# Optimization experiments

Hardware: AMD Instinct MI355X
Metric: run time of the kernel (lower is better)

Reference implementation:

```python
import jax, jax.numpy as jnp
import numpy as np

N = 50000
E = 800000
NFEAT = 128
NHID = 32
HEADS = 8
NCLASS = 40


def _gat_conv(x, src, dst, W, att_src, att_dst, bias, concat):
    # x: [N, Fin]; W: [Fin, H*C]; att_*: [H, C]; bias: [H*C] or [C]
    n = x.shape[0]
    H, C = att_src.shape
    h = (x @ W).reshape(n, H, C)                      # [N,H,C]
    a_src = (h * att_src[None]).sum(-1)               # [N,H]
    a_dst = (h * att_dst[None]).sum(-1)               # [N,H]
    e = jax.nn.leaky_relu(a_src[src] + a_dst[dst], 0.2)  # [E,H]
    # edge softmax over incoming edges of each dst node
    m = jax.ops.segment_max(e, dst, num_segments=n)   # [N,H]
    e = jnp.exp(e - m[dst])
    s = jax.ops.segment_sum(e, dst, num_segments=n)   # [N,H]
    alpha = e / (s[dst] + 1e-16)                      # [E,H]
    msg = h[src] * alpha[:, :, None]                  # [E,H,C]
    out = jax.ops.segment_sum(msg, dst, num_segments=n)  # [N,H,C]
    if concat:
        out = out.reshape(n, H * C)
    else:
        out = out.mean(axis=1)
    return out + bias


def setup_inputs() -> dict:
    key = jax.random.key(0)
    ks = jax.random.split(key, 10)
    x = jax.random.normal(ks[0], (N, NFEAT), dtype=jnp.float32)
    edge_index = jax.random.randint(ks[1], (2, E), 0, N, dtype=jnp.int64)
    sc = 1.0 / np.sqrt(NFEAT)
    W1 = jax.random.uniform(ks[2], (NFEAT, HEADS * NHID), jnp.float32, -sc, sc)
    a1_src = jax.random.uniform(ks[3], (HEADS, NHID), jnp.float32, -sc, sc)
    a1_dst = jax.random.uniform(ks[4], (HEADS, NHID), jnp.float32, -sc, sc)
    b1 = jnp.zeros((HEADS * NHID,), jnp.float32)
    sc2 = 1.0 / np.sqrt(HEADS * NHID)
    W2 = jax.random.uniform(ks[5], (HEADS * NHID, NCLASS), jnp.float32, -sc2, sc2)
    a2_src = jax.random.uniform(ks[6], (1, NCLASS), jnp.float32, -sc2, sc2)
    a2_dst = jax.random.uniform(ks[7], (1, NCLASS), jnp.float32, -sc2, sc2)
    b2 = jnp.zeros((NCLASS,), jnp.float32)
    return {"x": x, "edge_index": edge_index, "W1": W1, "a1_src": a1_src,
            "a1_dst": a1_dst, "b1": b1, "W2": W2, "a2_src": a2_src,
            "a2_dst": a2_dst, "b2": b2}


def reference(x, edge_index, W1, a1_src, a1_dst, b1, W2, a2_src, a2_dst, b2):
    n = x.shape[0]
    loop = jnp.arange(n, dtype=edge_index.dtype)
    src = jnp.concatenate([edge_index[0], loop])  # add self-loops (PyG default)
    dst = jnp.concatenate([edge_index[1], loop])
    # dropout layers are identity in eval mode
    h = jax.nn.elu(_gat_conv(x, src, dst, W1, a1_src, a1_dst, b1, concat=True))
    out = _gat_conv(h, src, dst, W2, a2_src, a2_dst, b2, concat=False)
    return jax.nn.log_softmax(out, axis=1)
```

## Files before the change

### kernel.cpp

```cpp
#include <hip/hip_runtime.h>
#include <math.h>

#define NFEAT  128
#define HC     256
#define HEADS  8
#define NHID   32
#define NCLASS 40

#define INV_LN2 1.44269504088896340736f

typedef unsigned int  uint;
typedef unsigned short ushort;
typedef unsigned char uchar;

typedef __attribute__((ext_vector_type(8))) short bf16x8;
typedef __attribute__((ext_vector_type(4))) float f32x4;

union U8 { uint4 u; bf16x8 v; };

__device__ __forceinline__ uint f2bf1(float f) {
    uint b = __float_as_uint(f);
    b += 0x7FFFu + ((b >> 16) & 1u);
    return b >> 16;
}
__device__ __forceinline__ uint packbf(float lo, float hi) {
    return f2bf1(lo) | (f2bf1(hi) << 16);
}

__device__ __forceinline__ uchar f2fp8(float v) {
    return (uchar)(__builtin_amdgcn_cvt_pk_fp8_f32(v, v, 0, false) & 0xFF);
}
__device__ __forceinline__ float fp8tof(uint byte) {
    auto v2 = __builtin_amdgcn_cvt_pk_f32_fp8((int)byte, false);
    return v2[0];
}

__device__ __forceinline__ float bperm(int addr, float v) {
    return __int_as_float(__builtin_amdgcn_ds_bpermute(addr, __float_as_int(v)));
}


#define HU 4
#define PREPB 23
__global__ __launch_bounds__(256)
void k_hist_prep(const int* __restrict__ srcE, const int* __restrict__ dstE,
                 int E, int* deg, int* __restrict__ srcs,
                 const float* __restrict__ W1,
                 const float* __restrict__ attS, const float* __restrict__ attD,
                 const float* __restrict__ W2,
                 const float* __restrict__ a2sw, const float* __restrict__ a2dw,
                 ushort* __restrict__ Wb1, ushort* __restrict__ Wb2) {
    int blk = blockIdx.x;
    int t = threadIdx.x;
    if (blk >= PREPB) {
        int tid = (blk - PREPB) * 256 + t;
        int stride = (gridDim.x - PREPB) * 256;
#pragma unroll
        for (int j = 0; j < HU; ++j) {
            int i = tid + j * stride;
            if (i < E) {
                int d = dstE[i];
                int slot = atomicAdd(&deg[d], 1);
                if (slot < 64) srcs[((size_t)d << 6) + slot] = srcE[i];
            }
        }
        return;
    }
    float f[8];
    if (blk < 17) {
        int g = blk * 256 + t;
        int lane = g & 63;
        int step = (g >> 6) & 3;
        int tile = g >> 8;
        int k0 = step * 32 + (lane >> 4) * 8;
        if (tile < 16) {
            int ncol = tile * 16 + (lane & 15);
#pragma unroll
            for (int j = 0; j < 8; ++j) f[j] = W1[(size_t)(k0 + j) * HC + ncol];
        } else {
            int cc = lane & 15;
            int h = cc & 7;
            const float* av = (cc < 8) ? attS : attD;
#pragma unroll
            for (int j = 0; j < 8; ++j) {
                const float* wr = W1 + (size_t)(k0 + j) * HC + h * 32;
                float s = 0.f;
#pragma unroll
                for (int c = 0; c < 32; ++c) s += wr[c] * av[h * 32 + c];
                f[j] = s * INV_LN2;
            }
        }
        uint4 o;
        o.x = packbf(f[0], f[1]);
        o.y = packbf(f[2], f[3]);
        o.z = packbf(f[4], f[5]);
        o.w = packbf(f[6], f[7]);
        *(uint4*)(Wb1 + (size_t)g * 8) = o;
    } else {
        int g = (blk - 17) * 256 + t;
        if (g >= 3 * 8 * 64) return;
        int lane = g & 63;
        int ks = (g >> 6) & 7;
        int nt = g >> 9;
        int cc = lane & 15;
        int ncol = nt * 16 + cc;
        int k0 = ks * 32 + (lane >> 4) * 8;
        if (ncol < NCLASS) {
#pragma unroll
            for (int j = 0; j < 8; ++j) f[j] = W2[(size_t)(k0 + j) * NCLASS + ncol];
        } else if (ncol <= 41) {
            const float* av = (ncol == 40) ? a2sw : a2dw;
#pragma unroll
            for (int j = 0; j < 8; ++j) {
                const float* wr = W2 + (size_t)(k0 + j) * NCLASS;
                float s = 0.f;
#pragma unroll
                for (int c = 0; c < NCLASS; ++c) s += wr[c] * av[c];
                f[j] = s * INV_LN2;
            }
        } else {
#pragma unroll
            for (int j = 0; j < 8; ++j) f[j] = 0.f;
        }
        uint4 o;
        o.x = packbf(f[0], f[1]);
        o.y = packbf(f[2], f[3]);
        o.z = packbf(f[4], f[5]);
        o.w = packbf(f[6], f[7]);
        *(uint4*)(Wb2 + (size_t)g * 8) = o;
    }
}

__global__ __launch_bounds__(256)
void k_gemm1(const float* __restrict__ x, const ushort* __restrict__ Wb,
             int n, uchar* __restrict__ h1f8, float* __restrict__ a1x) {
    __shared__ uint Xs[64 * 68];
    int t = threadIdx.x;
    int lane = t & 63;
    int w = t >> 6;
    int n0 = blockIdx.x * 64;

#pragma unroll
    for (int j = 0; j < 8; ++j) {
        int f4 = t + j * 256;
        int node = f4 >> 5;
        int k4 = (f4 & 31) * 4;
        int gn = n0 + node;
        float4 v = make_float4(0.f, 0.f, 0.f, 0.f);
        if (gn < n) v = *(const float4*)(x + (size_t)gn * NFEAT + k4);
        uint2 pk;
        pk.x = packbf(v.x, v.y);
        pk.y = packbf(v.z, v.w);
        *(uint2*)(Xs + node * 68 + (k4 >> 1)) = pk;
    }
    __syncthreads();

    int m = lane & 15;
    int q4 = (lane >> 4) * 4;
    bf16x8 Af[4];
#pragma unroll
    for (int ks = 0; ks < 4; ++ks) {
        U8 a;
        a.u = *(const uint4*)(Xs + (w * 16 + m) * 68 + ks * 16 + q4);
        Af[ks] = a.v;
    }
    __syncthreads();

    f32x4 acc[17];
#pragma unroll
    for (int i = 0; i < 17; ++i) acc[i] = (f32x4){0.f, 0.f, 0.f, 0.f};

    const bf16x8* Bf = (const bf16x8*)Wb;
#pragma unroll
    for (int ks = 0; ks < 4; ++ks) {
#pragma unroll
        for (int nt = 0; nt < 17; ++nt) {
            bf16x8 bv = Bf[(size_t)(nt * 4 + ks) * 64 + lane];
            acc[nt] = __builtin_amdgcn_mfma_f32_16x16x32_bf16(Af[ks], bv, acc[nt], 0, 0, 0);
        }
    }

    int cc = lane & 15;
    int r0 = (lane >> 4) * 4;

#pragma unroll
    for (int r = 0; r < 4; ++r) {
        int gn = n0 + w * 16 + r0 + r;
        if (gn < n) a1x[(size_t)gn * 16 + cc] = acc[16][r];
    }

    uchar* CsB = (uchar*)Xs;
#pragma unroll
    for (int nt = 0; nt < 16; ++nt) {
#pragma unroll
        for (int r = 0; r < 4; ++r)
            CsB[(w * 16 + r0 + r) * 272 + nt * 16 + cc] = f2fp8(acc[nt][r]);
    }
    __syncthreads();

    int node_local = t >> 2;
    int q = t & 3;
    int gn = n0 + node_local;
    if (gn < n) {
        const uchar* crow = CsB + node_local * 272 + q * 64;
        uchar* hp = h1f8 + (size_t)gn * HC + q * 64;
#pragma unroll
        for (int i = 0; i < 4; ++i)
            *(uint4*)(hp + i * 16) = *(const uint4*)(crow + i * 16);
    }
}

__global__ __launch_bounds__(256)
void k_agg1(const uint* __restrict__ h1u, const float* __restrict__ a1x,
            const float* __restrict__ b1, const int* __restrict__ deg,
            const int* __restrict__ srcs,
            int n, ushort* __restrict__ hgb) {
    int wid = blockIdx.x * 4 + (threadIdx.x >> 6);
    if (wid >= n) return;
    wid = __builtin_amdgcn_readfirstlane(wid);
    int lane = threadIdx.x & 63;
    int vj = lane >> 3;
    int hh = lane & 7;
    int hacc = lane >> 3;
    float adn = a1x[(size_t)wid * 16 + 8 + hh];
    const char* a1xb = (const char*)a1x;
    int ax8  = (lane ^ 8)  << 2;
    int ax16 = (lane ^ 16) << 2;
    int ax32 = (lane ^ 32) << 2;
    int bpc  = hacc << 2;
    int bpp[8];
#pragma unroll
    for (int j = 0; j < 8; ++j) bpp[j] = ((j << 3) + hacc) << 2;

    int degw = __builtin_amdgcn_readfirstlane(deg[wid]);
    degw = (degw < 63) ? degw : 63;
    int cnt = degw + 1;
    const int* srow = srcs + ((size_t)wid << 6);

    float s = 0.f;
    float4 acc = make_float4(0.f, 0.f, 0.f, 0.f);

    for (int i = 0; i < cnt; i += 8) {
        int idx = i + vj;
        int ldi = (idx < degw) ? idx : 0;
        int lv = srow[ldi];
        int sv = (idx < degw) ? lv : wid;
        bool valid = idx < cnt;
        float av = *(const float*)(a1xb + ((size_t)(uint)sv << 6) + ((uint)hh << 2));
        float a = av + adn;
        float e = fmaxf(a, 0.2f * a);
        float p = valid ? __builtin_exp2f(e) : 0.f;
        s += p;
#pragma unroll
        for (int j = 0; j < 8; ++j) {
            int snj = srow[i + j];
            snj = ((i + j) < degw) ? snj : wid;
            uint hv = h1u[(size_t)snj * 64 + lane];
            float pj = bperm(bpp[j], p);
            auto lo = __builtin_amdgcn_cvt_pk_f32_fp8((int)hv, false);
            auto hi = __builtin_amdgcn_cvt_pk_f32_fp8((int)hv, true);
            acc.x += pj * lo[0];
            acc.y += pj * lo[1];
            acc.z += pj * hi[0];
            acc.w += pj * hi[1];
        }
    }

    float ps = s + bperm(ax8, s);
    ps += bperm(ax16, ps);
    ps += bperm(ax32, ps);
    float inv = 1.f / (ps + 1e-16f);
    float inv_a = bperm(bpc, inv);
    float4 bv = *(const float4*)(b1 + lane * 4);
    float4 o;
    o.x = acc.x * inv_a + bv.x;
    o.y = acc.y * inv_a + bv.y;
    o.z = acc.z * inv_a + bv.z;
    o.w = acc.w * inv_a + bv.w;
    o.x = (o.x > 0.f) ? o.x : (__expf(o.x) - 1.f);
    o.y = (o.y > 0.f) ? o.y : (__expf(o.y) - 1.f);
    o.z = (o.z > 0.f) ? o.z : (__expf(o.z) - 1.f);
    o.w = (o.w > 0.f) ? o.w : (__expf(o.w) - 1.f);
    uint2 ov;
    ov.x = packbf(o.x, o.y);
    ov.y = packbf(o.z, o.w);
    *(uint2*)(hgb + (size_t)wid * HC + lane * 4) = ov;
}

__global__ __launch_bounds__(256)
void k_gemm2(const ushort* __restrict__ hgb, const ushort* __restrict__ Wb2,
             int n, uchar* __restrict__ h2f8) {
    __shared__ uint Xs[64 * 132];
    int t = threadIdx.x;
    int lane = t & 63;
    int w = t >> 6;
    int n0 = blockIdx.x * 64;

#pragma unroll
    for (int j = 0; j < 8; ++j) {
        int g = t + j * 256;
        int node = g >> 5;
        int u4 = g & 31;
        int gn = n0 + node;
        uint4 v = make_uint4(0u, 0u, 0u, 0u);
        if (gn < n) v = *(const uint4*)(hgb + (size_t)gn * HC + u4 * 8);
        *(uint4*)(Xs + node * 132 + u4 * 4) = v;
    }
    __syncthreads();

    int m = lane & 15;
    int q4 = (lane >> 4) * 4;
    bf16x8 Af[8];
#pragma unroll
    for (int ks = 0; ks < 8; ++ks) {
        U8 a;
        a.u = *(const uint4*)(Xs + (w * 16 + m) * 132 + ks * 16 + q4);
        Af[ks] = a.v;
    }
    __syncthreads();

    f32x4 acc[3];
#pragma unroll
    for (int i = 0; i < 3; ++i) acc[i] = (f32x4){0.f, 0.f, 0.f, 0.f};

    const bf16x8* Bf = (const bf16x8*)Wb2;
#pragma unroll
    for (int ks = 0; ks < 8; ++ks) {
#pragma unroll
        for (int nt = 0; nt < 3; ++nt) {
            bf16x8 bv = Bf[(size_t)(nt * 8 + ks) * 64 + lane];
            acc[nt] = __builtin_amdgcn_mfma_f32_16x16x32_bf16(Af[ks], bv, acc[nt], 0, 0, 0);
        }
    }

    int cc = lane & 15;
    int r0 = (lane >> 4) * 4;

    uchar* CsB = (uchar*)Xs;
#pragma unroll
    for (int nt = 0; nt < 2; ++nt) {
#pragma unroll
        for (int r = 0; r < 4; ++r)
            CsB[(w * 16 + r0 + r) * 64 + nt * 16 + cc] = f2fp8(acc[nt][r]);
    }
#pragma unroll
    for (int r = 0; r < 4; ++r) {
        int row = (w * 16 + r0 + r) * 64;
        if (cc < 8)       CsB[row + 32 + cc] = f2fp8(acc[2][r]);
        else if (cc == 8) *(float*)(CsB + row + 40) = acc[2][r];
        else if (cc == 9) *(float*)(CsB + row + 44) = acc[2][r];
        else if (cc == 10) *(uint*)(CsB + row + 48) = 0u;
        else if (cc == 11) *(uint*)(CsB + row + 52) = 0u;
        else if (cc == 12) *(uint*)(CsB + row + 56) = 0u;
        else if (cc == 13) *(uint*)(CsB + row + 60) = 0u;
    }
    __syncthreads();

    int node_local = t >> 2;
    int q = t & 3;
    int gn = n0 + node_local;
    if (gn < n)
        *(uint4*)(h2f8 + (size_t)gn * 64 + q * 16) =
            *(const uint4*)(CsB + node_local * 64 + q * 16);
}

__global__ __launch_bounds__(256)
void k_agg2(const uchar* __restrict__ h2f8, const float* __restrict__ b2,
            const int* __restrict__ deg, const int* __restrict__ srcs,
            int n, float* __restrict__ out) {
    int wid = blockIdx.x * 4 + (threadIdx.x >> 6);
    if (wid >= n) return;
    wid = __builtin_amdgcn_readfirstlane(wid);
    int lane = threadIdx.x & 63;
    int vj = lane & 7;
    bool live = lane < NCLASS;
    int col = live ? lane : 0;
    const char* h2b = (const char*)h2f8;
    float adn = *(const float*)(h2b + (size_t)wid * 64 + 44);
    int ax1 = (lane ^ 1) << 2;
    int ax2 = (lane ^ 2) << 2;
    int ax4 = (lane ^ 4) << 2;
    int bpj[8];
#pragma unroll
    for (int j = 0; j < 8; ++j) bpj[j] = j << 2;

    int degw = __builtin_amdgcn_readfirstlane(deg[wid]);
    degw = (degw < 63) ? degw : 63;
    int cnt = degw + 1;
    const int* srow = srcs + ((size_t)wid << 6);

    float s = 0.f, acc = 0.f;

    for (int i = 0; i < cnt; i += 8) {
        int idx = i + vj;
        int ldi = (idx < degw) ? idx : 0;
        int lv = srow[ldi];
        int sv = (idx < degw) ? lv : wid;
        bool valid = idx < cnt;
        float av = *(const float*)(h2b + ((size_t)(uint)sv << 6) + 40u);
        float a = av + adn;
        float e = fmaxf(a, 0.2f * a);
        float p = valid ? __builtin_exp2f(e) : 0.f;
        s += p;
#pragma unroll
        for (int j = 0; j < 8; ++j) {
            int snj = srow[i + j];
            snj = ((i + j) < degw) ? snj : wid;
            uint hb = h2f8[(size_t)snj * 64 + col];
            float pj = bperm(bpj[j], p);
            acc += pj * fp8tof(hb);
        }
    }

    float ps = s + bperm(ax1, s);
    ps += bperm(ax2, ps);
    ps += bperm(ax4, ps);

    float val0 = acc / (ps + 1e-16f) + (live ? b2[lane] : 0.f);
    float vmax = live ? val0 : -INFINITY;
#pragma unroll
    for (int msk = 1; msk < 64; msk <<= 1) vmax = fmaxf(vmax, __shfl_xor(vmax, msk, 64));
    float ex = live ? __expf(val0 - vmax) : 0.f;
#pragma unroll
    for (int msk = 1; msk < 64; msk <<= 1) ex += __shfl_xor(ex, msk, 64);
    float res = val0 - vmax - __logf(ex);
    if (live) out[(size_t)wid * NCLASS + lane] = res;
}

extern "C" void kernel_launch(void* const* d_in, const int* in_sizes, int n_in,
                              void* d_out, int out_size, void* d_ws, size_t ws_size,
                              hipStream_t stream) {
    const float* x    = (const float*)d_in[0];
    const int*   ei   = (const int*)  d_in[1];
    const float* W1   = (const float*)d_in[2];
    const float* attS = (const float*)d_in[3];
    const float* attD = (const float*)d_in[4];
    const float* b1   = (const float*)d_in[5];
    const float* W2   = (const float*)d_in[6];
    const float* a2sw = (const float*)d_in[7];
    const float* a2dw = (const float*)d_in[8];
    const float* b2   = (const float*)d_in[9];

    int n = in_sizes[0] / NFEAT;
    int E = in_sizes[1] / 2;
    const int* srcE = ei;
    const int* dstE = ei + E;
    int mblocks = (n + 63) / 64;

    char* p = (char*)d_ws;
    auto alloc = [&](size_t bytes) {
        char* r = p;
        p += (bytes + 255) & ~(size_t)255;
        return r;
    };
    uchar*  h1f8 = (uchar*)alloc((size_t)n * HC);
    ushort* hgb  = (ushort*)alloc((size_t)n * HC * 2);
    uchar*  h2f8 = (uchar*)alloc((size_t)n * 64);
    ushort* Wb1  = (ushort*)alloc((size_t)17 * 4 * 64 * 8 * 2);
    ushort* Wb2  = (ushort*)alloc((size_t)3 * 8 * 64 * 8 * 2);
    float* a1x = (float*)alloc((size_t)n * 16 * 4);
    int* deg  = (int*)alloc((size_t)n * 4);
    int* srcs = (int*)alloc((size_t)n * 64 * 4);

    int histb = (E + 256 * HU - 1) / (256 * HU);
    hipMemsetAsync(deg, 0, (size_t)n * 4, stream);
    k_hist_prep<<<PREPB + histb, 256, 0, stream>>>(srcE, dstE, E, deg, srcs,
                                                   W1, attS, attD, W2, a2sw, a2dw,
                                                   Wb1, Wb2);
    k_gemm1<<<mblocks, 256, 0, stream>>>(x, Wb1, n, h1f8, a1x);
    k_agg1<<<(n + 3) / 4, 256, 0, stream>>>((const uint*)h1f8, a1x, b1,
                                            deg, srcs, n, hgb);
    k_gemm2<<<mblocks, 256, 0, stream>>>(hgb, Wb2, n, h2f8);
    k_agg2<<<(n + 3) / 4, 256, 0, stream>>>(h2f8, b2, deg, srcs, n, (float*)d_out);
}
```

Baseline: 242.4 us.

## Split histogram into rank-count pass and scatter pass fused with GEMM1

The histogram kernel now only computes each edge's slot rank by atomic increment and stores it to a new rank array, instead of also writing the source index into the adjacency table. The scatter of source indices is moved into extra blocks of the first GEMM kernel, using vectorized int4 loads, so it runs concurrently with the feature transform. The intent is to shorten the atomic-bound histogram's dependency chain and hide the scatter behind GEMM work. In exchange it adds an extra E-sized int array that must be written and read back.

```diff
diff --git a/kernel.cpp b/kernel.cpp
--- a/kernel.cpp
+++ b/kernel.cpp
@@ -40,11 +40,11 @@
 }
 
 
-#define HU 4
+#define HU 8
 #define PREPB 23
 __global__ __launch_bounds__(256)
-void k_hist_prep(const int* __restrict__ srcE, const int* __restrict__ dstE,
-                 int E, int* deg, int* __restrict__ srcs,
+void k_hist_prep(const int* __restrict__ dst, int E, int* deg,
+                 int* __restrict__ rank,
                  const float* __restrict__ W1,
                  const float* __restrict__ attS, const float* __restrict__ attD,
                  const float* __restrict__ W2,
@@ -58,11 +58,7 @@
 #pragma unroll
         for (int j = 0; j < HU; ++j) {
             int i = tid + j * stride;
-            if (i < E) {
-                int d = dstE[i];
-                int slot = atomicAdd(&deg[d], 1);
-                if (slot < 64) srcs[((size_t)d << 6) + slot] = srcE[i];
-            }
+            if (i < E) rank[i] = atomicAdd(&deg[dst[i]], 1);
         }
         return;
     }
@@ -131,14 +127,44 @@
     }
 }
 
+#define SU 4
 __global__ __launch_bounds__(256)
-void k_gemm1(const float* __restrict__ x, const ushort* __restrict__ Wb,
-             int n, uchar* __restrict__ h1f8, float* __restrict__ a1x) {
+void k_scatter_gemm1(const int* __restrict__ srcE, const int* __restrict__ dstE,
+                     const int* __restrict__ rank, int E,
+                     int* __restrict__ srcs, int scb,
+                     const float* __restrict__ x, const ushort* __restrict__ Wb,
+                     int n, uchar* __restrict__ h1f8, float* __restrict__ a1x) {
     __shared__ uint Xs[64 * 68];
     int t = threadIdx.x;
+    if (blockIdx.x < scb) {
+        int tid = blockIdx.x * 256 + t;
+        int stride = scb * 256;
+        int P = (E + 3) >> 2;
+#pragma unroll
+        for (int g = 0; g < SU; ++g) {
+            int pk = tid + g * stride;
+            if (pk >= P) continue;
+            int i0 = pk * 4;
+            if (i0 + 4 <= E) {
+                int4 d4 = *(const int4*)(dstE + i0);
+                int4 r4 = *(const int4*)(rank + i0);
+                int4 s4 = *(const int4*)(srcE + i0);
+                if (r4.x < 64) srcs[((size_t)d4.x << 6) + r4.x] = s4.x;
+                if (r4.y < 64) srcs[((size_t)d4.y << 6) + r4.y] = s4.y;
+                if (r4.z < 64) srcs[((size_t)d4.z << 6) + r4.z] = s4.z;
+                if (r4.w < 64) srcs[((size_t)d4.w << 6) + r4.w] = s4.w;
+            } else {
+                for (int i = i0; i < E; ++i) {
+                    int r = rank[i];
+                    if (r < 64) srcs[((size_t)dstE[i] << 6) + r] = srcE[i];
+                }
+            }
+        }
+        return;
+    }
     int lane = t & 63;
     int w = t >> 6;
-    int n0 = blockIdx.x * 64;
+    int n0 = (blockIdx.x - scb) * 64;
 
 #pragma unroll
     for (int j = 0; j < 8; ++j) {
@@ -460,14 +486,18 @@
     ushort* Wb2  = (ushort*)alloc((size_t)3 * 8 * 64 * 8 * 2);
     float* a1x = (float*)alloc((size_t)n * 16 * 4);
     int* deg  = (int*)alloc((size_t)n * 4);
+    int* rank = (int*)alloc((size_t)E * 4);
     int* srcs = (int*)alloc((size_t)n * 64 * 4);
 
     int histb = (E + 256 * HU - 1) / (256 * HU);
+    int P = (E + 3) / 4;
+    int scb = (P + 256 * SU - 1) / (256 * SU);
     hipMemsetAsync(deg, 0, (size_t)n * 4, stream);
-    k_hist_prep<<<PREPB + histb, 256, 0, stream>>>(srcE, dstE, E, deg, srcs,
+    k_hist_prep<<<PREPB + histb, 256, 0, stream>>>(dstE, E, deg, rank,
                                                    W1, attS, attD, W2, a2sw, a2dw,
                                                    Wb1, Wb2);
-    k_gemm1<<<mblocks, 256, 0, stream>>>(x, Wb1, n, h1f8, a1x);
+    k_scatter_gemm1<<<scb + mblocks, 256, 0, stream>>>(
+        srcE, dstE, rank, E, srcs, scb, x, Wb1, n, h1f8, a1x);
     k_agg1<<<(n + 3) / 4, 256, 0, stream>>>((const uint*)h1f8, a1x, b1,
                                             deg, srcs, n, hgb);
     k_gemm2<<<mblocks, 256, 0, stream>>>(hgb, Wb2, n, h2f8);
```

Result: faster. 230.2 us (-5.0%).
